# Performance work log

Hardware: AMD Instinct MI355X
Metric: run time of the kernel (lower is better)

The kernel has to match this reference:

```python
import jax, jax.numpy as jnp
import numpy as np

N_TREE = 200
DEPTH = 3
N_LEAF = 2 ** (DEPTH + 1) - 1      # 15 internal decision nodes
N_LEAVES = N_LEAF + 1              # 16 leaves
N_NODE = 64
BATCH = 2048
D_FEAT = 512
LR = 0.01


def _leaf_paths(depth):
    """For each of the 2^(depth+1) leaves, the internal-node index and the
    left/right bit at every level (matches the tf.gather index construction:
    bit==0 -> take p, bit==1 -> take 1-p; children of node n are 2n+1, 2n+2)."""
    L = 2 ** (depth + 1)
    nodes = np.zeros((L, depth + 1), np.int32)
    bits = np.zeros((L, depth + 1), np.int32)
    for l in range(L):
        node = 0
        for d in range(depth + 1):
            bit = (l >> (depth - d)) & 1
            nodes[l, d] = node
            bits[l, d] = bit
            node = 2 * node + 1 + bit
    return nodes, bits

_NODES, _BITS = _leaf_paths(DEPTH)


def setup_inputs() -> dict:
    key = jax.random.key(0)
    ks = jax.random.split(key, 9)
    u = lambda k, s: jax.random.uniform(k, s, jnp.float32, -0.05, 0.05)  # keras 'uniform' init
    return {
        "x": jax.random.normal(ks[0], (BATCH, D_FEAT), jnp.float32),
        "y_true": jax.random.normal(ks[1], (BATCH, 1), jnp.float32),
        "w_t": u(ks[2], (N_TREE, D_FEAT, N_NODE)),
        "b_t": u(ks[3], (N_TREE, N_NODE)),
        "w_d": u(ks[4], (N_TREE, N_NODE, N_LEAF)),
        "b_d": u(ks[5], (N_TREE, N_LEAF)),
        "w_l": u(ks[6], (N_TREE, N_LEAVES)),
        "b_l": u(ks[7], (N_TREE,)),
        "f_0": jnp.full((1,), 0.5, jnp.float32),
    }


def reference(x, y_true, w_t, b_t, w_d, b_d, w_l, b_l, f_0):
    B = x.shape[0]
    # Batched per-tree small MLP (the 200-iteration Python loop in the original).
    # Dropout is identity at inference.
    h = jax.nn.relu(jnp.einsum('bd,tdn->tbn', x, w_t) + b_t[:, None, :])        # [T,B,N_NODE]
    p = jax.nn.sigmoid(jnp.einsum('tbn,tnl->tbl', h, w_d) + b_d[:, None, :])    # [T,B,15]
    # Soft binary-tree routing: mu[t,b,leaf] = prod over path of p or (1-p).
    # This reproduces the tiled-index tf.gather construction exactly.
    pn = p[..., _NODES]                                                         # [T,B,16,DEPTH+1]
    q = jnp.where(_BITS == 1, 1.0 - pn, pn)
    mu = jnp.prod(q, axis=-1)                                                   # [T,B,16]
    # Per-tree leaf score with tanh.
    f = jnp.tanh(jnp.einsum('tbl,tl->tb', mu, w_l) + b_l[:, None])              # [T,B]
    # Sequential boosting accumulation: predict_k = f_0 + lr * sum_{i<k} f_i.
    cum = f_0 + LR * jnp.cumsum(f.T, axis=1)                                    # [B,T]
    py_x = jnp.concatenate([jnp.broadcast_to(f_0[None, :], (B, 1)), cum], axis=1)  # [B,T+1]
    return py_x
```

## Files before the change

kernel.cpp:

```cpp
#include <hip/hip_runtime.h>

#define T_TREES 200
#define BATCH   2048
#define D_FEAT  512
#define N_NODE  64
#define LR      0.01f

typedef __attribute__((__ext_vector_type__(8)))  __bf16 bf16x8;
typedef __attribute__((__ext_vector_type__(16))) float  f32x16;

__device__ __forceinline__ unsigned short f32_to_bf16(float f) {
    unsigned u = __float_as_uint(f);
    u += 0x7FFFu + ((u >> 16) & 1u);
    return (unsigned short)(u >> 16);
}

__device__ __forceinline__ void gload_lds16(const void* g, void* l) {
    __builtin_amdgcn_global_load_lds(
        (__attribute__((address_space(1))) void*)(void*)g,
        (__attribute__((address_space(3))) void*)l,
        16, 0, 0);
}


__global__ __launch_bounds__(256) void prep_x(const float* __restrict__ x,
                                              unsigned short* __restrict__ x_p) {
    __shared__ float tile[64 * 65];
    int mb = blockIdx.x >> 3;
    int slab = blockIdx.x & 7;
    const float* src = x + (mb * 64) * D_FEAT + slab * 64;
    #pragma unroll
    for (int p = 0; p < 16; ++p) {
        int idx = p * 256 + threadIdx.x;
        int r = idx >> 6, c = idx & 63;
        tile[r * 65 + c] = src[r * D_FEAT + c];
    }
    __syncthreads();
    int mt = mb >> 2, mq = mb & 3;
    unsigned short* dst = x_p + mt * 131072 + slab * 8 * 2048 + mq * 64 * 8;
    #pragma unroll
    for (int p = 0; p < 8; ++p) {
        int idx = p * 256 + threadIdx.x;
        int kgl = idx >> 8;
        int r   = (idx >> 2) & 63;
        int jp  = idx & 3;
        ushort2 o;
        o.x = f32_to_bf16(tile[r * 65 + kgl * 8 + jp * 2]);
        o.y = f32_to_bf16(tile[r * 65 + kgl * 8 + jp * 2 + 1]);
        *(ushort2*)(dst + kgl * 2048 + r * 8 + jp * 2) = o;
    }
}

__global__ __launch_bounds__(256) void prep_wt(const float* __restrict__ w_t,
                                               unsigned short* __restrict__ w_p) {
    __shared__ float tile[64 * 65];
    int t = blockIdx.x >> 3, slab = blockIdx.x & 7;
    const float* src = w_t + t * (D_FEAT * N_NODE) + slab * 64 * N_NODE;
    #pragma unroll
    for (int p = 0; p < 16; ++p) {
        int idx = p * 256 + threadIdx.x;
        int d = idx >> 6, n = idx & 63;
        tile[d * 65 + n] = src[d * N_NODE + n];
    }
    __syncthreads();
    unsigned short* dst = w_p + (t >> 1) * 65536 + slab * 8 * 1024 + (t & 1) * 64 * 8;
    #pragma unroll
    for (int p = 0; p < 8; ++p) {
        int idx = p * 256 + threadIdx.x;
        int kgl = idx >> 8;
        int n   = (idx >> 2) & 63;
        int jp  = idx & 3;
        ushort2 o;
        o.x = f32_to_bf16(tile[(kgl * 8 + jp * 2) * 65 + n]);
        o.y = f32_to_bf16(tile[(kgl * 8 + jp * 2 + 1) * 65 + n]);
        *(ushort2*)(dst + kgl * 1024 + n * 8 + jp * 2) = o;
    }
}

__global__ void prep_wd(const float* __restrict__ w_d, unsigned short* __restrict__ w_dt) {
    int i = blockIdx.x * 256 + threadIdx.x;
    int n = i & 63;
    int l = (i >> 6) & 31;
    int t = i >> 11;
    float v = (l < 15) ? w_d[(t * 64 + n) * 15 + l] : 0.f;
    w_dt[i] = f32_to_bf16(v);
}

__global__ __launch_bounds__(256, 2) void gbdt_main(
    const unsigned short* __restrict__ x_p,
    const unsigned short* __restrict__ w_p,
    const unsigned short* __restrict__ w_dt,
    const float* __restrict__ b_t,
    const float* __restrict__ b_d,
    const float* __restrict__ w_l,
    const float* __restrict__ b_l,
    float* __restrict__ f_ws)
{
    __shared__ alignas(16) char smem[49152];
    unsigned short* H  = (unsigned short*)smem;
    float*          Pf = (float*)smem;

    const int tid    = threadIdx.x;
    const int lane   = tid & 63;
    const int w      = tid >> 6;
    const int lane31 = lane & 31;
    const int kh     = lane >> 5;
    const int wm     = w >> 1;
    const int wn     = w & 1;

    const int xcd  = blockIdx.x & 7;
    const int slot = blockIdx.x >> 3;
    const int mt   = slot & 7;
    const int pj   = slot >> 3;
    const int pair = xcd * 13 + pj;
    if (pair >= 100) return;
    const int t0 = pair * 2;
    const int m0 = mt * 256;

    const char* pa = (const char*)(x_p + mt * 131072) + tid * 16;
    const char* pb = (const char*)(w_p + pair * 65536) + tid * 16;

    f32x16 acc[4][2];
    #pragma unroll
    for (int mb = 0; mb < 4; ++mb)
        #pragma unroll
        for (int nb = 0; nb < 2; ++nb)
            acc[mb][nb] = (f32x16)(0.f);

    #pragma unroll
    for (int i = 0; i < 4; ++i)
        gload_lds16(pa + i * 4096, smem + tid * 16 + i * 4096);
    #pragma unroll
    for (int i = 0; i < 2; ++i)
        gload_lds16(pb + i * 4096, smem + 16384 + tid * 16 + i * 4096);

    const int aoff = (wm * 128 + lane31) * 16;
    const int boff = 16384 + (wn * 64 + lane31) * 16;

    for (int c = 0; c < 16; ++c) {
        __syncthreads();
        if (c < 15) {
            char* nx = smem + ((c + 1) & 1) * 24576;
            #pragma unroll
            for (int i = 0; i < 4; ++i)
                gload_lds16(pa + (c + 1) * 16384 + i * 4096, nx + tid * 16 + i * 4096);
            #pragma unroll
            for (int i = 0; i < 2; ++i)
                gload_lds16(pb + (c + 1) * 8192 + i * 4096, nx + 16384 + tid * 16 + i * 4096);
        }
        const char* buf = smem + (c & 1) * 24576;
        #pragma unroll
        for (int s2 = 0; s2 < 2; ++s2) {
            const int kgl = 2 * s2 + kh;
            bf16x8 av[4], bv[2];
            #pragma unroll
            for (int mb = 0; mb < 4; ++mb)
                av[mb] = *(const bf16x8*)(buf + aoff + kgl * 4096 + mb * 512);
            #pragma unroll
            for (int nb = 0; nb < 2; ++nb)
                bv[nb] = *(const bf16x8*)(buf + boff + kgl * 2048 + nb * 512);
            #pragma unroll
            for (int mb = 0; mb < 4; ++mb)
                #pragma unroll
                for (int nb = 0; nb < 2; ++nb)
                    acc[mb][nb] = __builtin_amdgcn_mfma_f32_32x32x16_bf16(
                        av[mb], bv[nb], acc[mb][nb], 0, 0, 0);
        }
    }

    __syncthreads();

    float btv[2];
    #pragma unroll
    for (int nb = 0; nb < 2; ++nb)
        btv[nb] = b_t[(t0 + wn) * 64 + nb * 32 + lane31];

    f32x16 acc2[2][2];
    #pragma unroll
    for (int j = 0; j < 2; ++j) {
        if (wn == j) {
            #pragma unroll
            for (int mb = 0; mb < 4; ++mb)
                #pragma unroll
                for (int nb = 0; nb < 2; ++nb)
                    #pragma unroll
                    for (int r = 0; r < 16; ++r) {
                        int m  = wm * 128 + mb * 32 + (r & 3) + 8 * (r >> 2) + 4 * kh;
                        int cl = nb * 32 + lane31;
                        float h = fmaxf(acc[mb][nb][r] + btv[nb], 0.f);
                        H[m * 72 + cl] = f32_to_bf16(h);
                    }
        }
        __syncthreads();
        #pragma unroll
        for (int i = 0; i < 2; ++i) acc2[j][i] = (f32x16)(0.f);
        const unsigned short* pW = w_dt + (t0 + j) * 2048 + lane31 * 64;
        #pragma unroll
        for (int s2 = 0; s2 < 4; ++s2) {
            int kg2 = 2 * s2 + kh;
            bf16x8 bv = *(const bf16x8*)(pW + kg2 * 8);
            #pragma unroll
            for (int i = 0; i < 2; ++i) {
                int mrow = (w * 2 + i) * 32 + lane31;
                bf16x8 av = *(const bf16x8*)(H + mrow * 72 + kg2 * 8);
                acc2[j][i] = __builtin_amdgcn_mfma_f32_32x32x16_bf16(av, bv, acc2[j][i], 0, 0, 0);
            }
        }
        __syncthreads();
    }

    float bdv[2];
    #pragma unroll
    for (int j = 0; j < 2; ++j)
        bdv[j] = (lane31 < 15) ? b_d[(t0 + j) * 15 + lane31] : 0.f;
    if (lane31 < 15) {
        #pragma unroll
        for (int j = 0; j < 2; ++j)
            #pragma unroll
            for (int i = 0; i < 2; ++i)
                #pragma unroll
                for (int r = 0; r < 16; ++r) {
                    int m = (w * 2 + i) * 32 + (r & 3) + 8 * (r >> 2) + 4 * kh;
                    float lg = acc2[j][i][r] + bdv[j];
                    Pf[(j * 256 + m) * 17 + lane31] = 1.f / (1.f + __expf(-lg));
                }
    }
    __syncthreads();

    {
        int m = tid;
        #pragma unroll
        for (int j = 0; j < 2; ++j) {
            int t = t0 + j;
            float pv[15];
            #pragma unroll
            for (int i = 0; i < 15; ++i) pv[i] = Pf[(j * 256 + m) * 17 + i];
            float facc = 0.f;
            #pragma unroll
            for (int leaf = 0; leaf < 16; ++leaf) {
                float mu = 1.f;
                int node = 0;
                #pragma unroll
                for (int d = 0; d < 4; ++d) {
                    int bit = (leaf >> (3 - d)) & 1;
                    float p = pv[node];
                    mu *= bit ? (1.f - p) : p;
                    node = 2 * node + 1 + bit;
                }
                facc += mu * w_l[t * 16 + leaf];
            }
            f_ws[(m0 + m) * T_TREES + t] = tanhf(facc + b_l[t]);
        }
    }
}

__global__ void scan_k(const float* __restrict__ f_ws, const float* __restrict__ f0p,
                       float* __restrict__ out) {
    int b = blockIdx.x, tid = threadIdx.x;
    int lane = tid & 63, wid = tid >> 6;
    float f0 = f0p[0];
    float x = (tid < T_TREES) ? f_ws[b * T_TREES + tid] : 0.f;
    #pragma unroll
    for (int off = 1; off < 64; off <<= 1) {
        float y = __shfl_up(x, off, 64);
        if (lane >= off) x += y;
    }
    __shared__ float wsum[4];
    if (lane == 63) wsum[wid] = x;
    __syncthreads();
    float base = 0.f;
    for (int i = 0; i < wid; ++i) base += wsum[i];
    float incl = x + base;
    if (tid == 0) out[b * (T_TREES + 1)] = f0;
    if (tid < T_TREES) out[b * (T_TREES + 1) + 1 + tid] = f0 + LR * incl;
}

extern "C" void kernel_launch(void* const* d_in, const int* in_sizes, int n_in,
                              void* d_out, int out_size, void* d_ws, size_t ws_size,
                              hipStream_t stream) {
    const float* x   = (const float*)d_in[0];
    const float* w_t = (const float*)d_in[2];
    const float* b_t = (const float*)d_in[3];
    const float* w_d = (const float*)d_in[4];
    const float* b_d = (const float*)d_in[5];
    const float* w_l = (const float*)d_in[6];
    const float* b_l = (const float*)d_in[7];
    const float* f_0 = (const float*)d_in[8];
    float* out = (float*)d_out;

    char* ws = (char*)d_ws;
    unsigned short* x_p  = (unsigned short*)(ws);
    unsigned short* w_p  = (unsigned short*)(ws + 2097152);
    unsigned short* w_dt = (unsigned short*)(ws + 15204352);
    float*          f_ws = (float*)(ws + 16023552);

    prep_x  <<< 256, 256, 0, stream>>>(x, x_p);
    prep_wt <<<1600, 256, 0, stream>>>(w_t, w_p);
    prep_wd <<<1600, 256, 0, stream>>>(w_d, w_dt);
    gbdt_main<<<832, 256, 0, stream>>>(x_p, w_p, w_dt, b_t, b_d, w_l, b_l, f_ws);
    scan_k<<<BATCH, 256, 0, stream>>>(f_ws, f_0, out);
}
```

Measured before the change: 141.9 us.

## Halve batch tile per block and process both trees' second layer concurrently

The batch tile per block drops from 256 to 128 rows, so twice as many blocks launch. LDS shrinks to 36 KB and launch bounds allow 3 blocks per CU. The x packing layout changes to match. The second-layer MFMA now runs both trees at once, with each wave pair handling one tree from a separate H buffer, which removes the serialized per-tree loop and its extra barriers. The cost is that each weight tile is reloaded twice as often, and each block does less MFMA work to amortize its fixed overhead.

Result: faster. 134.1 us (-5.5%).

```diff
diff --git a/kernel.cpp b/kernel.cpp
--- a/kernel.cpp
+++ b/kernel.cpp
@@ -36,8 +36,8 @@
         tile[r * 65 + c] = src[r * D_FEAT + c];
     }
     __syncthreads();
-    int mt = mb >> 2, mq = mb & 3;
-    unsigned short* dst = x_p + mt * 131072 + slab * 8 * 2048 + mq * 64 * 8;
+    int mt = mb >> 1, mq = mb & 1;
+    unsigned short* dst = x_p + mt * 65536 + slab * 8192 + mq * 512;
     #pragma unroll
     for (int p = 0; p < 8; ++p) {
         int idx = p * 256 + threadIdx.x;
@@ -47,7 +47,7 @@
         ushort2 o;
         o.x = f32_to_bf16(tile[r * 65 + kgl * 8 + jp * 2]);
         o.y = f32_to_bf16(tile[r * 65 + kgl * 8 + jp * 2 + 1]);
-        *(ushort2*)(dst + kgl * 2048 + r * 8 + jp * 2) = o;
+        *(ushort2*)(dst + kgl * 1024 + r * 8 + jp * 2) = o;
     }
 }
 
@@ -63,7 +63,7 @@
         tile[d * 65 + n] = src[d * N_NODE + n];
     }
     __syncthreads();
-    unsigned short* dst = w_p + (t >> 1) * 65536 + slab * 8 * 1024 + (t & 1) * 64 * 8;
+    unsigned short* dst = w_p + (t >> 1) * 65536 + slab * 8192 + (t & 1) * 512;
     #pragma unroll
     for (int p = 0; p < 8; ++p) {
         int idx = p * 256 + threadIdx.x;
@@ -86,7 +86,7 @@
     w_dt[i] = f32_to_bf16(v);
 }
 
-__global__ __launch_bounds__(256, 2) void gbdt_main(
+__global__ __launch_bounds__(256, 3) void gbdt_main(
     const unsigned short* __restrict__ x_p,
     const unsigned short* __restrict__ w_p,
     const unsigned short* __restrict__ w_dt,
@@ -96,8 +96,8 @@
     const float* __restrict__ b_l,
     float* __restrict__ f_ws)
 {
-    __shared__ alignas(16) char smem[49152];
-    unsigned short* H  = (unsigned short*)smem;
+    __shared__ alignas(16) char smem[36864];
+    unsigned short* Hs = (unsigned short*)smem;
     float*          Pf = (float*)smem;
 
     const int tid    = threadIdx.x;
@@ -110,57 +110,55 @@
 
     const int xcd  = blockIdx.x & 7;
     const int slot = blockIdx.x >> 3;
-    const int mt   = slot & 7;
-    const int pj   = slot >> 3;
+    const int mt   = slot & 15;
+    const int pj   = slot >> 4;
     const int pair = xcd * 13 + pj;
     if (pair >= 100) return;
     const int t0 = pair * 2;
-    const int m0 = mt * 256;
-
-    const char* pa = (const char*)(x_p + mt * 131072) + tid * 16;
-    const char* pb = (const char*)(w_p + pair * 65536) + tid * 16;
-
-    f32x16 acc[4][2];
-    #pragma unroll
-    for (int mb = 0; mb < 4; ++mb)
+    const int m0 = mt * 128;
+
+    const char* ga = (const char*)(x_p + mt * 65536) + tid * 16;
+    const char* gb = (const char*)(w_p + pair * 65536) + tid * 16;
+
+    f32x16 acc[2][2];
+    #pragma unroll
+    for (int mb = 0; mb < 2; ++mb)
         #pragma unroll
         for (int nb = 0; nb < 2; ++nb)
             acc[mb][nb] = (f32x16)(0.f);
 
     #pragma unroll
-    for (int i = 0; i < 4; ++i)
-        gload_lds16(pa + i * 4096, smem + tid * 16 + i * 4096);
-    #pragma unroll
-    for (int i = 0; i < 2; ++i)
-        gload_lds16(pb + i * 4096, smem + 16384 + tid * 16 + i * 4096);
-
-    const int aoff = (wm * 128 + lane31) * 16;
-    const int boff = 16384 + (wn * 64 + lane31) * 16;
+    for (int i = 0; i < 2; ++i) {
+        gload_lds16(ga + i * 4096, smem + tid * 16 + i * 4096);
+        gload_lds16(gb + i * 4096, smem + 8192 + tid * 16 + i * 4096);
+    }
+
+    const int aoff = (wm * 64 + lane31) * 16;
+    const int boff = 8192 + (wn * 64 + lane31) * 16;
 
     for (int c = 0; c < 16; ++c) {
         __syncthreads();
         if (c < 15) {
-            char* nx = smem + ((c + 1) & 1) * 24576;
-            #pragma unroll
-            for (int i = 0; i < 4; ++i)
-                gload_lds16(pa + (c + 1) * 16384 + i * 4096, nx + tid * 16 + i * 4096);
-            #pragma unroll
-            for (int i = 0; i < 2; ++i)
-                gload_lds16(pb + (c + 1) * 8192 + i * 4096, nx + 16384 + tid * 16 + i * 4096);
-        }
-        const char* buf = smem + (c & 1) * 24576;
+            char* nx = smem + ((c + 1) & 1) * 16384;
+            #pragma unroll
+            for (int i = 0; i < 2; ++i) {
+                gload_lds16(ga + (c + 1) * 8192 + i * 4096, nx + tid * 16 + i * 4096);
+                gload_lds16(gb + (c + 1) * 8192 + i * 4096, nx + 8192 + tid * 16 + i * 4096);
+            }
+        }
+        const char* buf = smem + (c & 1) * 16384;
         #pragma unroll
         for (int s2 = 0; s2 < 2; ++s2) {
             const int kgl = 2 * s2 + kh;
-            bf16x8 av[4], bv[2];
-            #pragma unroll
-            for (int mb = 0; mb < 4; ++mb)
-                av[mb] = *(const bf16x8*)(buf + aoff + kgl * 4096 + mb * 512);
+            bf16x8 av[2], bv[2];
+            #pragma unroll
+            for (int mb = 0; mb < 2; ++mb)
+                av[mb] = *(const bf16x8*)(buf + aoff + kgl * 2048 + mb * 512);
             #pragma unroll
             for (int nb = 0; nb < 2; ++nb)
                 bv[nb] = *(const bf16x8*)(buf + boff + kgl * 2048 + nb * 512);
             #pragma unroll
-            for (int mb = 0; mb < 4; ++mb)
+            for (int mb = 0; mb < 2; ++mb)
                 #pragma unroll
                 for (int nb = 0; nb < 2; ++nb)
                     acc[mb][nb] = __builtin_amdgcn_mfma_f32_32x32x16_bf16(
@@ -170,87 +168,70 @@
 
     __syncthreads();
 
-    float btv[2];
-    #pragma unroll
-    for (int nb = 0; nb < 2; ++nb)
-        btv[nb] = b_t[(t0 + wn) * 64 + nb * 32 + lane31];
-
-    f32x16 acc2[2][2];
-    #pragma unroll
-    for (int j = 0; j < 2; ++j) {
-        if (wn == j) {
-            #pragma unroll
-            for (int mb = 0; mb < 4; ++mb)
-                #pragma unroll
-                for (int nb = 0; nb < 2; ++nb)
-                    #pragma unroll
-                    for (int r = 0; r < 16; ++r) {
-                        int m  = wm * 128 + mb * 32 + (r & 3) + 8 * (r >> 2) + 4 * kh;
-                        int cl = nb * 32 + lane31;
-                        float h = fmaxf(acc[mb][nb][r] + btv[nb], 0.f);
-                        H[m * 72 + cl] = f32_to_bf16(h);
-                    }
-        }
-        __syncthreads();
-        #pragma unroll
-        for (int i = 0; i < 2; ++i) acc2[j][i] = (f32x16)(0.f);
-        const unsigned short* pW = w_dt + (t0 + j) * 2048 + lane31 * 64;
-        #pragma unroll
-        for (int s2 = 0; s2 < 4; ++s2) {
-            int kg2 = 2 * s2 + kh;
-            bf16x8 bv = *(const bf16x8*)(pW + kg2 * 8);
-            #pragma unroll
-            for (int i = 0; i < 2; ++i) {
-                int mrow = (w * 2 + i) * 32 + lane31;
-                bf16x8 av = *(const bf16x8*)(H + mrow * 72 + kg2 * 8);
-                acc2[j][i] = __builtin_amdgcn_mfma_f32_32x32x16_bf16(av, bv, acc2[j][i], 0, 0, 0);
-            }
-        }
-        __syncthreads();
-    }
-
-    float bdv[2];
-    #pragma unroll
-    for (int j = 0; j < 2; ++j)
-        bdv[j] = (lane31 < 15) ? b_d[(t0 + j) * 15 + lane31] : 0.f;
+    #pragma unroll
+    for (int nb = 0; nb < 2; ++nb) {
+        float btv = b_t[(t0 + wn) * 64 + nb * 32 + lane31];
+        #pragma unroll
+        for (int mb = 0; mb < 2; ++mb)
+            #pragma unroll
+            for (int r = 0; r < 16; ++r) {
+                int m = wm * 64 + mb * 32 + (r & 3) + 8 * (r >> 2) + 4 * kh;
+                float h = fmaxf(acc[mb][nb][r] + btv, 0.f);
+                Hs[wn * 8704 + m * 68 + nb * 32 + lane31] = f32_to_bf16(h);
+            }
+    }
+    __syncthreads();
+
+    f32x16 acc2[2] = { (f32x16)(0.f), (f32x16)(0.f) };
+    const unsigned short* pW = w_dt + (t0 + wn) * 2048 + lane31 * 64 + kh * 8;
+    #pragma unroll
+    for (int s = 0; s < 4; ++s) {
+        bf16x8 bv = *(const bf16x8*)(pW + s * 16);
+        #pragma unroll
+        for (int i = 0; i < 2; ++i) {
+            const unsigned short* pH =
+                Hs + wn * 8704 + (wm * 64 + i * 32 + lane31) * 68 + s * 16 + kh * 8;
+            bf16x8 av = *(const bf16x8*)pH;
+            acc2[i] = __builtin_amdgcn_mfma_f32_32x32x16_bf16(av, bv, acc2[i], 0, 0, 0);
+        }
+    }
+    __syncthreads();
+
     if (lane31 < 15) {
-        #pragma unroll
-        for (int j = 0; j < 2; ++j)
-            #pragma unroll
-            for (int i = 0; i < 2; ++i)
-                #pragma unroll
-                for (int r = 0; r < 16; ++r) {
-                    int m = (w * 2 + i) * 32 + (r & 3) + 8 * (r >> 2) + 4 * kh;
-                    float lg = acc2[j][i][r] + bdv[j];
-                    Pf[(j * 256 + m) * 17 + lane31] = 1.f / (1.f + __expf(-lg));
-                }
+        float bdv = b_d[(t0 + wn) * 15 + lane31];
+        #pragma unroll
+        for (int i = 0; i < 2; ++i)
+            #pragma unroll
+            for (int r = 0; r < 16; ++r) {
+                int m = wm * 64 + i * 32 + (r & 3) + 8 * (r >> 2) + 4 * kh;
+                float lg = acc2[i][r] + bdv;
+                Pf[(wn * 128 + m) * 17 + lane31] = 1.f / (1.f + __expf(-lg));
+            }
     }
     __syncthreads();
 
     {
-        int m = tid;
-        #pragma unroll
-        for (int j = 0; j < 2; ++j) {
-            int t = t0 + j;
-            float pv[15];
-            #pragma unroll
-            for (int i = 0; i < 15; ++i) pv[i] = Pf[(j * 256 + m) * 17 + i];
-            float facc = 0.f;
-            #pragma unroll
-            for (int leaf = 0; leaf < 16; ++leaf) {
-                float mu = 1.f;
-                int node = 0;
-                #pragma unroll
-                for (int d = 0; d < 4; ++d) {
-                    int bit = (leaf >> (3 - d)) & 1;
-                    float p = pv[node];
-                    mu *= bit ? (1.f - p) : p;
-                    node = 2 * node + 1 + bit;
-                }
-                facc += mu * w_l[t * 16 + leaf];
-            }
-            f_ws[(m0 + m) * T_TREES + t] = tanhf(facc + b_l[t]);
-        }
+        int m = tid & 127;
+        int j = tid >> 7;
+        int t = t0 + j;
+        float pv[15];
+        #pragma unroll
+        for (int i = 0; i < 15; ++i) pv[i] = Pf[(j * 128 + m) * 17 + i];
+        float facc = 0.f;
+        #pragma unroll
+        for (int leaf = 0; leaf < 16; ++leaf) {
+            float mu = 1.f;
+            int node = 0;
+            #pragma unroll
+            for (int d = 0; d < 4; ++d) {
+                int bit = (leaf >> (3 - d)) & 1;
+                float p = pv[node];
+                mu *= bit ? (1.f - p) : p;
+                node = 2 * node + 1 + bit;
+            }
+            facc += mu * w_l[t * 16 + leaf];
+        }
+        f_ws[(m0 + m) * T_TREES + t] = tanhf(facc + b_l[t]);
     }
 }
 
@@ -297,6 +278,6 @@
     prep_x  <<< 256, 256, 0, stream>>>(x, x_p);
     prep_wt <<<1600, 256, 0, stream>>>(w_t, w_p);
     prep_wd <<<1600, 256, 0, stream>>>(w_d, w_dt);
-    gbdt_main<<<832, 256, 0, stream>>>(x_p, w_p, w_dt, b_t, b_d, w_l, b_l, f_ws);
+    gbdt_main<<<1664, 256, 0, stream>>>(x_p, w_p, w_dt, b_t, b_d, w_l, b_l, f_ws);
     scan_k<<<BATCH, 256, 0, stream>>>(f_ws, f_0, out);
 }
```
